# Kernel optimization log

Hardware: AMD Instinct MI355X
Metric: run time of the kernel (lower is better)

The kernel has to match this reference:

```python
import jax, jax.numpy as jnp
import numpy as np

B, C, T, H, W = 32, 512, 16, 14, 14
DS = 7
HW = H * W
STD = 0.03


def setup_inputs() -> dict:
    key = jax.random.key(0)
    ks = jax.random.split(key, 6)
    x_in = jax.random.normal(ks[0], (B, C, T, HW), jnp.float32)
    # nn.Linear weights stored as (in, out) so forward is x @ W + b
    W1 = jax.random.truncated_normal(ks[1], -2.0, 2.0, (DS * DS * C, C), jnp.float32) * STD
    b1 = jnp.zeros((C,), jnp.float32)
    W2 = jax.random.truncated_normal(ks[2], -2.0, 2.0, (C, C // 8), jnp.float32) * STD
    b2 = jnp.zeros((C // 8,), jnp.float32)
    Wa = jax.random.truncated_normal(ks[3], -2.0, 2.0, (T * T, T // 2), jnp.float32) * STD
    Wd = jax.random.truncated_normal(ks[4], -2.0, 2.0, (T * T, T // 2), jnp.float32) * STD
    return {"x_in": x_in, "W1": W1, "b1": b1, "W2": W2, "b2": b2, "Wa": Wa, "Wd": Wd}


def _temporal_sample(x_in, idx):
    # Faithful to F.grid_sample(bilinear, padding_mode='border', align_corners=False)
    # on a (b, hw*c, t, 1) tensor: the width axis is size 1 and the grid x-coord is 0,
    # which maps exactly to pixel 0 with full weight, so only the t-axis matters.
    # normalize_grid uses n-1 = t-1; unnormalize (align_corners=False) gives:
    #   pixel = ((norm + 1) * t - 1) / 2 = idx * t / (t - 1) - 0.5
    b, c, t, hw = x_in.shape
    p = idx * (t / (t - 1)) - 0.5            # (b, t//2)
    i0 = jnp.floor(p)
    w = (p - i0)[:, None, :, None]           # (b, 1, t//2, 1)
    i0i = i0.astype(jnp.int32)
    i0c = jnp.clip(i0i, 0, t - 1)[:, None, :, None]
    i1c = jnp.clip(i0i + 1, 0, t - 1)[:, None, :, None]
    g0 = jnp.take_along_axis(x_in, jnp.broadcast_to(i0c, (b, c, t // 2, hw)), axis=2)
    g1 = jnp.take_along_axis(x_in, jnp.broadcast_to(i1c, (b, c, t // 2, hw)), axis=2)
    return (1.0 - w) * g0 + w * g1           # (b, c, t//2, hw)


def reference(x_in, W1, b1, W2, b2, Wa, Wd):
    b, c, t, hw = x_in.shape
    # (b, c, t, hw) -> (b, t, c, H, W)
    xi = x_in.reshape(b, c, t, H, W).transpose(0, 2, 1, 3, 4)
    # adaptive_avg_pool2d 14x14 -> 7x7 is an exact 2x2 mean
    xi = xi.reshape(b, t, c, DS, 2, DS, 2).mean(axis=(4, 6))      # (b, t, c, 7, 7)
    xi = xi.transpose(0, 1, 3, 4, 2).reshape(b, t, DS * DS * c)    # (b, t, 25088)
    h = jax.nn.gelu(xi @ W1 + b1, approximate=False)
    feat = h @ W2 + b2                                             # (b, t, c//8)
    scaler = 1.0 / c
    attn = jax.nn.softmax(scaler * jnp.einsum('btd,bsd->bts', feat, feat), axis=-1)
    flat = attn.reshape(b, t * t)
    receptive_field = 2.0
    off_a = jnp.tanh(flat @ Wa) * receptive_field                  # (b, t//2)
    off_d = jnp.tanh(flat @ Wd) * receptive_field
    idx_a = jnp.arange(0, t, 2, dtype=x_in.dtype)[None, :] + off_a
    idx_d = jnp.arange(1, t, 2, dtype=x_in.dtype)[None, :] + off_d
    x_a = _temporal_sample(x_in, idx_a)
    x_d = _temporal_sample(x_in, idx_d)
    return x_a, x_d
```

## Files before the change

kernel.cpp:

```cpp
#include <hip/hip_runtime.h>
#include <math.h>

#define CC 512
#define K1 25088
#define N1 512
#define NE 25690112

typedef unsigned short ushort_t;
typedef __attribute__((ext_vector_type(8))) short bf16x8;
typedef __attribute__((ext_vector_type(4))) float f32x4;
typedef __attribute__((address_space(3))) void* as3_void;
typedef const __attribute__((address_space(1))) void* as1_cvoid;

__device__ __forceinline__ ushort_t f2bf(float f) {
  union { float f; unsigned u; } v; v.f = f;
  unsigned r = v.u + 0x7fffu + ((v.u >> 16) & 1u);
  return (ushort_t)(r >> 16);
}

__global__ void k_w1t(const float* __restrict__ W1, ushort_t* __restrict__ W1t) {
  __shared__ float tile[32][33];
  int k0 = blockIdx.x * 32;
  int n0 = blockIdx.y * 32;
  int tx = threadIdx.x & 31, ty = threadIdx.x >> 5;
  for (int r = 0; r < 32; r += 8)
    tile[ty + r][tx] = W1[(k0 + ty + r) * N1 + n0 + tx];
  __syncthreads();
  for (int r = 0; r < 32; r += 8)
    W1t[(size_t)(n0 + ty + r) * K1 + k0 + tx] = f2bf(tile[tx][ty + r]);
}

__global__ void k_pool(const float* __restrict__ x, ushort_t* __restrict__ A) {
  int tid = blockIdx.x * 256 + threadIdx.x;
  int c = tid & 511;
  int r = tid >> 9;
  int i = r % 7;
  int r2 = r / 7;
  int t = r2 & 15;
  int b = r2 >> 4;
  const float* src = x + ((size_t)(b * 512 + c) * 16 + t) * 196;
  int bt = b * 16 + t;
  ushort_t* dst = A + (size_t)bt * K1 + i * 7 * 512 + c;
  int h0 = 2 * i * 14;
  for (int j = 0; j < 7; ++j) {
    float2 a0 = *(const float2*)(src + h0 + 2 * j);
    float2 a1 = *(const float2*)(src + h0 + 14 + 2 * j);
    dst[j * 512] = f2bf((a0.x + a0.y + a1.x + a1.y) * 0.25f);
  }
}

__global__ __launch_bounds__(256)
void k_gemm1(const ushort_t* __restrict__ A, const ushort_t* __restrict__ Bt,
             float* __restrict__ C) {
  __shared__ __align__(16) short As[4][128][8];
  __shared__ __align__(16) short Bs[4][128][8];
  int row0 = blockIdx.x * 128;
  int col0 = blockIdx.y * 128;
  int k0 = blockIdx.z * 512;
  int lane = threadIdx.x & 63;
  int wave = threadIdx.x >> 6;
  int wm = (wave & 1) * 64;
  int wn = (wave >> 1) * 64;
  f32x4 acc[4][4] = {};

  for (int kk = 0; kk < 512; kk += 32) {
    __syncthreads();
    for (int t = 0; t < 2; ++t) {
      int wt = wave * 2 + t;
      int ch = wt >> 1;
      int r0 = (wt & 1) * 64;
      int rr = r0 + lane;
      const ushort_t* ga = A  + (size_t)(row0 + rr) * K1 + (k0 + kk + ch * 8);
      const ushort_t* gb = Bt + (size_t)(col0 + rr) * K1 + (k0 + kk + ch * 8);
      __builtin_amdgcn_global_load_lds((as1_cvoid)ga, (as3_void)&As[ch][r0][0], 16, 0, 0);
      __builtin_amdgcn_global_load_lds((as1_cvoid)gb, (as3_void)&Bs[ch][r0][0], 16, 0, 0);
    }
    __syncthreads();
    int ml = lane & 15, q = lane >> 4;
    bf16x8 af[4], bfr[4];
    for (int sm = 0; sm < 4; ++sm)
      af[sm] = *(const bf16x8*)&As[q][wm + sm * 16 + ml][0];
    for (int sn = 0; sn < 4; ++sn)
      bfr[sn] = *(const bf16x8*)&Bs[q][wn + sn * 16 + ml][0];
    for (int sm = 0; sm < 4; ++sm)
      for (int sn = 0; sn < 4; ++sn)
        acc[sm][sn] = __builtin_amdgcn_mfma_f32_16x16x32_bf16(af[sm], bfr[sn], acc[sm][sn], 0, 0, 0);
  }
  int ml = lane & 15, q = lane >> 4;
  for (int sm = 0; sm < 4; ++sm)
    for (int sn = 0; sn < 4; ++sn)
      for (int rg = 0; rg < 4; ++rg) {
        int row = row0 + wm + sm * 16 + q * 4 + rg;
        int col = col0 + wn + sn * 16 + ml;
        atomicAdd(&C[row * N1 + col], acc[sm][sn][rg]);
      }
}

__global__ void k_biasgelu(const float* __restrict__ C, const float* __restrict__ b1,
                           float* __restrict__ h) {
  int i = blockIdx.x * 256 + threadIdx.x;
  float x = C[i] + b1[i & 511];
  h[i] = 0.5f * x * (1.0f + erff(x * 0.70710678118654752f));
}

__global__ void k_gemm2(const float* __restrict__ h, const float* __restrict__ W2,
                        const float* __restrict__ b2, float* __restrict__ feat) {
  int bt = blockIdx.x;
  int n = threadIdx.x;
  __shared__ float hs[512];
  for (int k = threadIdx.x; k < 512; k += 64) hs[k] = h[bt * 512 + k];
  __syncthreads();
  float acc = b2[n];
  for (int k = 0; k < 512; ++k) acc += hs[k] * W2[k * 64 + n];
  feat[bt * 64 + n] = acc;
}

__global__ void k_attn(const float* __restrict__ feat, const float* __restrict__ Wa,
                       const float* __restrict__ Wd, float* __restrict__ offs) {
  int b = blockIdx.x;
  __shared__ float fl[1024];
  __shared__ float lg[256];
  int tid = threadIdx.x;
  for (int i = tid; i < 1024; i += 256) fl[i] = feat[b * 1024 + i];
  __syncthreads();
  {
    int t = tid >> 4, s = tid & 15;
    float a = 0.f;
    for (int d = 0; d < 64; ++d) a += fl[t * 64 + d] * fl[s * 64 + d];
    lg[tid] = a * (1.0f / 512.0f);
  }
  __syncthreads();
  if (tid < 16) {
    float m = -1e30f;
    for (int s = 0; s < 16; ++s) m = fmaxf(m, lg[tid * 16 + s]);
    float e[16], sum = 0.f;
    for (int s = 0; s < 16; ++s) { e[s] = expf(lg[tid * 16 + s] - m); sum += e[s]; }
    float inv = 1.0f / sum;
    for (int s = 0; s < 16; ++s) lg[tid * 16 + s] = e[s] * inv;
  }
  __syncthreads();
  if (tid < 16) {
    int which = tid >> 3, col = tid & 7;
    const float* W = which ? Wd : Wa;
    float a = 0.f;
    for (int f = 0; f < 256; ++f) a += lg[f] * W[f * 8 + col];
    offs[b * 16 + tid] = tanhf(a) * 2.0f;
  }
}

__global__ void k_sample(const float* __restrict__ x, const float* __restrict__ offs,
                         float* __restrict__ out) {
  int bc = blockIdx.x;
  int b = bc >> 9;
  __shared__ float4 xs[16 * 49];
  __shared__ int i0s[16], i1s[16];
  __shared__ float wfr[16];
  int tid = threadIdx.x;
  const float4* src = (const float4*)(x + (size_t)bc * 16 * 196);
  for (int i = tid; i < 784; i += 256) xs[i] = src[i];
  if (tid < 16) {
    int which = tid >> 3, to = tid & 7;
    float idx = (float)(2 * to + which) + offs[b * 16 + tid];
    float p = idx * (16.0f / 15.0f) - 0.5f;
    float fl = floorf(p);
    int i0 = (int)fl;
    wfr[tid] = p - fl;
    i0s[tid] = min(max(i0, 0), 15);
    i1s[tid] = min(max(i0 + 1, 0), 15);
  }
  __syncthreads();
  float4* out4 = (float4*)out;
  for (int oi = tid; oi < 784; oi += 256) {
    int which = oi / 392;
    int rem = oi - which * 392;
    int to = rem / 49;
    int q = rem - to * 49;
    int slot = which * 8 + to;
    float w = wfr[slot];
    float4 g0 = xs[i0s[slot] * 49 + q];
    float4 g1 = xs[i1s[slot] * 49 + q];
    float4 o;
    o.x = g0.x + w * (g1.x - g0.x);
    o.y = g0.y + w * (g1.y - g0.y);
    o.z = g0.z + w * (g1.z - g0.z);
    o.w = g0.w + w * (g1.w - g0.w);
    out4[(size_t)which * (NE / 4) + (size_t)(bc * 8 + to) * 49 + q] = o;
  }
}

extern "C" void kernel_launch(void* const* d_in, const int* in_sizes, int n_in,
                              void* d_out, int out_size, void* d_ws, size_t ws_size,
                              hipStream_t stream) {
  const float* x  = (const float*)d_in[0];
  const float* W1 = (const float*)d_in[1];
  const float* b1 = (const float*)d_in[2];
  const float* W2 = (const float*)d_in[3];
  const float* b2 = (const float*)d_in[4];
  const float* Wa = (const float*)d_in[5];
  const float* Wd = (const float*)d_in[6];
  float* out = (float*)d_out;

  char* w = (char*)d_ws;
  ushort_t* Abf  = (ushort_t*)(w);
  ushort_t* W1t  = (ushort_t*)(w + 25690112);
  float*    C1   = (float*)(w + 51380224);
  float*    h    = (float*)(w + 52428800);
  float*    feat = (float*)(w + 53477376);
  float*    offs = (float*)(w + 53608448);

  hipMemsetAsync(C1, 0, 1048576, stream);
  k_w1t<<<dim3(784, 16), 256, 0, stream>>>(W1, W1t);
  k_pool<<<7168, 256, 0, stream>>>(x, Abf);
  k_gemm1<<<dim3(4, 4, 49), 256, 0, stream>>>(Abf, W1t, C1);
  k_biasgelu<<<1024, 256, 0, stream>>>(C1, b1, h);
  k_gemm2<<<512, 64, 0, stream>>>(h, W2, b2, feat);
  k_attn<<<32, 256, 0, stream>>>(feat, Wa, Wd, offs);
  k_sample<<<16384, 256, 0, stream>>>(x, offs, out);
}
```

Baseline: 552.3 us.

## Coalesce pool and transpose, replace split-K atomics with partial buffers, fuse head

The pooling kernel now stages 64 channels of a (b,t) slice in shared memory with float4 loads and writes bf16 output coalesced along channels. The W1 transpose uses 64x64 tiles with vector loads and 4-wide stores. The split-K GEMM writes 49 partial tiles to a workspace instead of using atomics, and a reduce kernel sums them and applies bias and GELU, which removes the memset. GEMM2, attention and offset computation are fused into one per-batch kernel. The trade-off is about 51MB of extra partial-sum traffic in place of atomic contention.

```diff
diff --git a/kernel.cpp b/kernel.cpp
--- a/kernel.cpp
+++ b/kernel.cpp
@@ -12,46 +12,77 @@
 typedef __attribute__((address_space(3))) void* as3_void;
 typedef const __attribute__((address_space(1))) void* as1_cvoid;
 
+struct us4 { ushort_t a, b, c, d; };
+
 __device__ __forceinline__ ushort_t f2bf(float f) {
   union { float f; unsigned u; } v; v.f = f;
   unsigned r = v.u + 0x7fffu + ((v.u >> 16) & 1u);
   return (ushort_t)(r >> 16);
 }
 
-__global__ void k_w1t(const float* __restrict__ W1, ushort_t* __restrict__ W1t) {
-  __shared__ float tile[32][33];
-  int k0 = blockIdx.x * 32;
-  int n0 = blockIdx.y * 32;
-  int tx = threadIdx.x & 31, ty = threadIdx.x >> 5;
-  for (int r = 0; r < 32; r += 8)
-    tile[ty + r][tx] = W1[(k0 + ty + r) * N1 + n0 + tx];
-  __syncthreads();
-  for (int r = 0; r < 32; r += 8)
-    W1t[(size_t)(n0 + ty + r) * K1 + k0 + tx] = f2bf(tile[tx][ty + r]);
-}
-
-__global__ void k_pool(const float* __restrict__ x, ushort_t* __restrict__ A) {
-  int tid = blockIdx.x * 256 + threadIdx.x;
-  int c = tid & 511;
-  int r = tid >> 9;
-  int i = r % 7;
-  int r2 = r / 7;
-  int t = r2 & 15;
-  int b = r2 >> 4;
-  const float* src = x + ((size_t)(b * 512 + c) * 16 + t) * 196;
-  int bt = b * 16 + t;
-  ushort_t* dst = A + (size_t)bt * K1 + i * 7 * 512 + c;
-  int h0 = 2 * i * 14;
-  for (int j = 0; j < 7; ++j) {
-    float2 a0 = *(const float2*)(src + h0 + 2 * j);
-    float2 a1 = *(const float2*)(src + h0 + 14 + 2 * j);
-    dst[j * 512] = f2bf((a0.x + a0.y + a1.x + a1.y) * 0.25f);
+__global__ __launch_bounds__(256)
+void k_w1t(const float* __restrict__ W1, ushort_t* __restrict__ W1t) {
+  __shared__ float tile[64][65];
+  int k0 = blockIdx.x * 64;
+  int n0 = blockIdx.y * 64;
+  int tid = threadIdx.x;
+  int rg = tid >> 4;
+  int m  = tid & 15;
+  for (int it = 0; it < 4; ++it) {
+    int row = rg + it * 16;
+    float4 v = *(const float4*)&W1[(size_t)(k0 + row) * N1 + n0 + m * 4];
+    tile[row][m * 4 + 0] = v.x;
+    tile[row][m * 4 + 1] = v.y;
+    tile[row][m * 4 + 2] = v.z;
+    tile[row][m * 4 + 3] = v.w;
+  }
+  __syncthreads();
+  for (int it = 0; it < 4; ++it) {
+    int n = rg + it * 16;
+    int kb = m * 4;
+    us4 o;
+    o.a = f2bf(tile[kb + 0][n]);
+    o.b = f2bf(tile[kb + 1][n]);
+    o.c = f2bf(tile[kb + 2][n]);
+    o.d = f2bf(tile[kb + 3][n]);
+    *(us4*)&W1t[(size_t)(n0 + n) * K1 + k0 + kb] = o;
+  }
+}
+
+__global__ __launch_bounds__(256)
+void k_pool(const float* __restrict__ x, ushort_t* __restrict__ A) {
+  __shared__ float s[64][197];
+  int bx = blockIdx.x;
+  int cch = bx & 7;
+  int t = (bx >> 3) & 15;
+  int b = bx >> 7;
+  int c0 = cch * 64;
+  int tid = threadIdx.x;
+  for (int idx = tid; idx < 3136; idx += 256) {
+    int c = idx / 49;
+    int q = idx - c * 49;
+    float4 v = *(const float4*)&x[(((size_t)(b * 512 + c0 + c) * 16) + t) * 196 + q * 4];
+    s[c][q * 4 + 0] = v.x;
+    s[c][q * 4 + 1] = v.y;
+    s[c][q * 4 + 2] = v.z;
+    s[c][q * 4 + 3] = v.w;
+  }
+  __syncthreads();
+  ushort_t* dst = A + (size_t)(b * 16 + t) * K1 + c0;
+  for (int o = tid; o < 3136; o += 256) {
+    int ij = o >> 6;
+    int c = o & 63;
+    int i = ij / 7;
+    int j = ij - i * 7;
+    int pos = i * 28 + j * 2;
+    float v = (s[c][pos] + s[c][pos + 1] + s[c][pos + 14] + s[c][pos + 15]) * 0.25f;
+    dst[ij * 512 + c] = f2bf(v);
   }
 }
 
 __global__ __launch_bounds__(256)
 void k_gemm1(const ushort_t* __restrict__ A, const ushort_t* __restrict__ Bt,
-             float* __restrict__ C) {
+             float* __restrict__ Cp) {
   __shared__ __align__(16) short As[4][128][8];
   __shared__ __align__(16) short Bs[4][128][8];
   int row0 = blockIdx.x * 128;
@@ -87,46 +118,59 @@
         acc[sm][sn] = __builtin_amdgcn_mfma_f32_16x16x32_bf16(af[sm], bfr[sn], acc[sm][sn], 0, 0, 0);
   }
   int ml = lane & 15, q = lane >> 4;
+  float* out = Cp + (size_t)blockIdx.z * 262144;
   for (int sm = 0; sm < 4; ++sm)
     for (int sn = 0; sn < 4; ++sn)
       for (int rg = 0; rg < 4; ++rg) {
         int row = row0 + wm + sm * 16 + q * 4 + rg;
         int col = col0 + wn + sn * 16 + ml;
-        atomicAdd(&C[row * N1 + col], acc[sm][sn][rg]);
+        out[row * N1 + col] = acc[sm][sn][rg];
       }
 }
 
-__global__ void k_biasgelu(const float* __restrict__ C, const float* __restrict__ b1,
-                           float* __restrict__ h) {
+__global__ __launch_bounds__(256)
+void k_reduce(const float* __restrict__ Cp, const float* __restrict__ b1,
+              float* __restrict__ h) {
   int i = blockIdx.x * 256 + threadIdx.x;
-  float x = C[i] + b1[i & 511];
-  h[i] = 0.5f * x * (1.0f + erff(x * 0.70710678118654752f));
-}
-
-__global__ void k_gemm2(const float* __restrict__ h, const float* __restrict__ W2,
-                        const float* __restrict__ b2, float* __restrict__ feat) {
-  int bt = blockIdx.x;
-  int n = threadIdx.x;
-  __shared__ float hs[512];
-  for (int k = threadIdx.x; k < 512; k += 64) hs[k] = h[bt * 512 + k];
-  __syncthreads();
-  float acc = b2[n];
-  for (int k = 0; k < 512; ++k) acc += hs[k] * W2[k * 64 + n];
-  feat[bt * 64 + n] = acc;
-}
-
-__global__ void k_attn(const float* __restrict__ feat, const float* __restrict__ Wa,
-                       const float* __restrict__ Wd, float* __restrict__ offs) {
+  float a = 0.f;
+  for (int z = 0; z < 49; ++z) a += Cp[(size_t)z * 262144 + i];
+  float xv = a + b1[i & 511];
+  h[i] = 0.5f * xv * (1.0f + erff(xv * 0.70710678118654752f));
+}
+
+__global__ __launch_bounds__(256)
+void k_head(const float* __restrict__ h, const float* __restrict__ W2,
+            const float* __restrict__ b2, const float* __restrict__ Wa,
+            const float* __restrict__ Wd, float* __restrict__ offs) {
   int b = blockIdx.x;
-  __shared__ float fl[1024];
+  __shared__ float hs[16][512];
+  __shared__ float fl[16][65];
   __shared__ float lg[256];
   int tid = threadIdx.x;
-  for (int i = tid; i < 1024; i += 256) fl[i] = feat[b * 1024 + i];
+  for (int idx = tid; idx < 8192; idx += 256)
+    hs[idx >> 9][idx & 511] = h[(size_t)b * 8192 + idx];
+  __syncthreads();
+  {
+    int n = tid & 63;
+    int tg = tid >> 6;
+    float acc0 = b2[n], acc1 = acc0, acc2 = acc0, acc3 = acc0;
+    for (int k = 0; k < 512; ++k) {
+      float w = W2[k * 64 + n];
+      acc0 += hs[tg][k] * w;
+      acc1 += hs[tg + 4][k] * w;
+      acc2 += hs[tg + 8][k] * w;
+      acc3 += hs[tg + 12][k] * w;
+    }
+    fl[tg][n] = acc0;
+    fl[tg + 4][n] = acc1;
+    fl[tg + 8][n] = acc2;
+    fl[tg + 12][n] = acc3;
+  }
   __syncthreads();
   {
     int t = tid >> 4, s = tid & 15;
     float a = 0.f;
-    for (int d = 0; d < 64; ++d) a += fl[t * 64 + d] * fl[s * 64 + d];
+    for (int d = 0; d < 64; ++d) a += fl[t][d] * fl[s][d];
     lg[tid] = a * (1.0f / 512.0f);
   }
   __syncthreads();
@@ -148,8 +192,9 @@
   }
 }
 
-__global__ void k_sample(const float* __restrict__ x, const float* __restrict__ offs,
-                         float* __restrict__ out) {
+__global__ __launch_bounds__(256)
+void k_sample(const float* __restrict__ x, const float* __restrict__ offs,
+              float* __restrict__ out) {
   int bc = blockIdx.x;
   int b = bc >> 9;
   __shared__ float4 xs[16 * 49];
@@ -203,17 +248,16 @@
   char* w = (char*)d_ws;
   ushort_t* Abf  = (ushort_t*)(w);
   ushort_t* W1t  = (ushort_t*)(w + 25690112);
-  float*    C1   = (float*)(w + 51380224);
-  float*    h    = (float*)(w + 52428800);
-  float*    feat = (float*)(w + 53477376);
-  float*    offs = (float*)(w + 53608448);
-
-  hipMemsetAsync(C1, 0, 1048576, stream);
-  k_w1t<<<dim3(784, 16), 256, 0, stream>>>(W1, W1t);
-  k_pool<<<7168, 256, 0, stream>>>(x, Abf);
-  k_gemm1<<<dim3(4, 4, 49), 256, 0, stream>>>(Abf, W1t, C1);
-  k_biasgelu<<<1024, 256, 0, stream>>>(C1, b1, h);
-  k_gemm2<<<512, 64, 0, stream>>>(h, W2, b2, feat);
-  k_attn<<<32, 256, 0, stream>>>(feat, Wa, Wd, offs);
+  float*    Cp   = (float*)(w + 51380224);
+  float*    h    = (float*)(w + 51380224 + 51380224);
+  float*    feat_offs = (float*)(w + 51380224 + 51380224 + 1048576);
+
+  float* offs = feat_offs;
+
+  k_w1t<<<dim3(392, 8), 256, 0, stream>>>(W1, W1t);
+  k_pool<<<4096, 256, 0, stream>>>(x, Abf);
+  k_gemm1<<<dim3(4, 4, 49), 256, 0, stream>>>(Abf, W1t, Cp);
+  k_reduce<<<1024, 256, 0, stream>>>(Cp, b1, h);
+  k_head<<<32, 256, 0, stream>>>(h, W2, b2, Wa, Wd, offs);
   k_sample<<<16384, 256, 0, stream>>>(x, offs, out);
 }
```

After: 547.4 us. Within noise of the previous version (-0.9%).
